# Performance work log

Measured on AMD Instinct MI355X. Metric: run time of the kernel, lower is better.

Reference implementation:

```python
import jax, jax.numpy as jnp
import numpy as np

# J6 incidence matrix for Plucker coordinates (constant buffer in the torch module)
_J6 = jnp.array([[0, 0, 0, 0, 0, 1],
                 [0, 0, 0, 0, -1, 0],
                 [0, 0, 0, 1, 0, 0],
                 [0, 0, 1, 0, 0, 0],
                 [0, -1, 0, 0, 0, 0],
                 [1, 0, 0, 0, 0, 0]], dtype=jnp.float32)

# combinations(range(4), 2) index pairs for the exterior product
_PI = np.array([0, 0, 0, 1, 1, 2])
_PJ = np.array([1, 2, 3, 2, 3, 3])


def plucker_lines(p1, p2):
    # p1, p2: (..., 4) -> normalized Plucker 6-vectors (..., 6)
    lines = p1[..., _PI] * p2[..., _PJ] - p1[..., _PJ] * p2[..., _PI]
    n = jnp.linalg.norm(lines, axis=-1, keepdims=True)
    return lines / jnp.maximum(n, 1e-12)


def setup_inputs() -> dict:
    key = jax.random.key(0)
    ks = jax.random.split(key, 6)
    B, T, D, H = 1, 2048, 1024, 16
    s = D ** -0.5
    x = jax.random.normal(ks[0], (B, T, D), jnp.float32)
    Wqkv = jax.random.normal(ks[1], (D, 3 * D), jnp.float32) * s
    bqkv = jnp.zeros((3 * D,), jnp.float32)
    W1p = jax.random.normal(ks[2], (D, 4 * H), jnp.float32) * s
    W2p = jax.random.normal(ks[3], (D, 4 * H), jnp.float32) * s
    plucker_scale = jnp.full((H,), 0.1, jnp.float32)
    Wout = jax.random.normal(ks[4], (D, D), jnp.float32) * s
    bout = jnp.zeros((D,), jnp.float32)
    return {"x": x, "Wqkv": Wqkv, "bqkv": bqkv, "W1p": W1p, "W2p": W2p,
            "plucker_scale": plucker_scale, "Wout": Wout, "bout": bout}


def reference(x, Wqkv, bqkv, W1p, W2p, plucker_scale, Wout, bout):
    B, T, D = x.shape
    H = plucker_scale.shape[0]
    dh = D // H

    qkv = (x @ Wqkv + bqkv).reshape(B, T, 3, H, dh)
    q = jnp.transpose(qkv[:, :, 0], (0, 2, 1, 3))  # [B,H,T,dh]
    k = jnp.transpose(qkv[:, :, 1], (0, 2, 1, 3))
    v = jnp.transpose(qkv[:, :, 2], (0, 2, 1, 3))

    std_logits = jnp.einsum('bhid,bhjd->bhij', q, k) * (dh ** -0.5)

    p1 = (x @ W1p).reshape(B, T, H, 4)
    p2 = (x @ W2p).reshape(B, T, H, 4)
    lines_h = jnp.transpose(plucker_lines(p1, p2), (0, 2, 1, 3))  # [B,H,T,6]
    Jlines = lines_h @ _J6.T                                       # [B,H,T,6]
    plucker_bias = jnp.einsum('bhic,bhjc->bhij', lines_h, Jlines)  # [B,H,T,T]

    logits = std_logits + plucker_bias * plucker_scale[None, :, None, None]
    causal = jnp.triu(jnp.ones((T, T), bool), 1)
    logits = jnp.where(causal[None, None], -jnp.inf, logits)
    attn = jax.nn.softmax(logits, axis=-1)

    out = jnp.einsum('bhij,bhjd->bhid', attn, v)
    out = jnp.transpose(out, (0, 2, 1, 3)).reshape(B, T, D)
    return out @ Wout + bout
```

## Files before the change

kernel.cpp:

```cpp
#include <hip/hip_runtime.h>

typedef unsigned short u16;
typedef unsigned int u32;
typedef __attribute__((ext_vector_type(8))) __bf16 bf16x8;
typedef __attribute__((ext_vector_type(4))) float f32x4;
typedef __attribute__((ext_vector_type(4))) u16 u16x4;

#define MFMA16(a, b, c) __builtin_amdgcn_mfma_f32_16x16x32_bf16((a), (b), (c), 0, 0, 0)

static __device__ __forceinline__ u16 f2b(float f) {
  union { float f; u32 u; } v; v.f = f;
  u32 u = v.u;
  return (u16)((u + 0x7FFFu + ((u >> 16) & 1u)) >> 16);
}

static __device__ __forceinline__ u32 pack2(float a, float b) {
  u32 r;
  asm("v_cvt_pk_bf16_f32 %0, %1, %2" : "=v"(r) : "v"(a), "v"(b));
  return r;
}

static __device__ __forceinline__ float exp2fast(float x) {
#if defined(__has_builtin) && __has_builtin(__builtin_amdgcn_exp2f)
  return __builtin_amdgcn_exp2f(x);
#else
  return __expf(x * 0.6931471805599453f);
#endif
}

static __device__ __forceinline__ void gload16(const u16* gp, u16* lp) {
  __builtin_amdgcn_global_load_lds((__attribute__((address_space(1))) void*)(u16*)gp,
                                   (__attribute__((address_space(3))) void*)lp, 16, 0, 0);
}

__global__ __launch_bounds__(256) void k_prep(const float* __restrict__ Wqkv, const float* __restrict__ Wout,
                                              const float* __restrict__ W1p, const float* __restrict__ W2p,
                                              const float* __restrict__ x,
                                              u16* __restrict__ WB, u16* __restrict__ WoT,
                                              u16* __restrict__ xb) {
  const int b = blockIdx.x;
  const int t = threadIdx.x;
  if (b < 4096) {
    __shared__ float tile[32][33];
    const float* src; u16* dst; int N, n0, k0;
    if (b < 3072) { src = Wqkv; dst = WB;  N = 3072; n0 = (b % 96) * 32; k0 = (b / 96) * 32; }
    else { const int bb = b - 3072; src = Wout; dst = WoT; N = 1024; n0 = (bb & 31) * 32; k0 = (bb >> 5) * 32; }
    const int r = t >> 3, c4 = (t & 7) << 2;
    const float4 in4 = *(const float4*)(src + (size_t)(k0 + r) * N + n0 + c4);
    tile[r][c4 + 0] = in4.x; tile[r][c4 + 1] = in4.y;
    tile[r][c4 + 2] = in4.z; tile[r][c4 + 3] = in4.w;
    __syncthreads();
    u16x4 o;
    o.x = f2b(tile[c4 + 0][r]); o.y = f2b(tile[c4 + 1][r]);
    o.z = f2b(tile[c4 + 2][r]); o.w = f2b(tile[c4 + 3][r]);
    *(u16x4*)(dst + (size_t)(n0 + r) * 1024 + k0 + c4) = o;
  } else if (b < 4608) {
    const int idx = (b - 4096) * 256 + t;
    const int j = idx >> 10, k = idx & 1023;
    const float v = (j < 64) ? W1p[(size_t)k * 64 + j] : W2p[(size_t)k * 64 + (j - 64)];
    WB[(size_t)3072 * 1024 + idx] = f2b(v);
  } else {
    const size_t idx = ((size_t)(b - 4608) * 256 + t) << 2;
    const float4 v = *(const float4*)(x + idx);
    u16x4 o; o.x = f2b(v.x); o.y = f2b(v.y); o.z = f2b(v.z); o.w = f2b(v.w);
    *(u16x4*)(xb + idx) = o;
  }
}

static __device__ __forceinline__ void gemm_core_128x64(const u16* __restrict__ A, const u16* __restrict__ B,
                                                        int brow, int bcol, int K,
                                                        u16* ldsA, u16* ldsB, f32x4 acc[4][2]) {
  const int tid = threadIdx.x;
  const int wave = tid >> 6, lane = tid & 63;
  const int wr = wave >> 1, wc = wave & 1;
  const int g = lane >> 4, l15 = lane & 15;

  for (int k0 = 0; k0 < K; k0 += 64) {
#pragma unroll
    for (int li = 0; li < 4; ++li) {
      const int f = li * 256 + wave * 64 + lane;
      const int row = f >> 3;
      const int slot = f & 7;
      const int gcol = ((slot ^ (row & 7)) << 3);
      gload16(A + (size_t)(brow + row) * K + k0 + gcol, ldsA + (size_t)(li * 256 + wave * 64) * 8);
    }
#pragma unroll
    for (int li = 0; li < 2; ++li) {
      const int f = li * 256 + wave * 64 + lane;
      const int row = f >> 3;
      const int slot = f & 7;
      const int gcol = ((slot ^ (row & 7)) << 3);
      gload16(B + (size_t)(bcol + row) * K + k0 + gcol, ldsB + (size_t)(li * 256 + wave * 64) * 8);
    }
    __syncthreads();
    bf16x8 af[4][2], bfr[2][2];
#pragma unroll
    for (int kk = 0; kk < 2; ++kk) {
#pragma unroll
      for (int m = 0; m < 4; ++m) {
        const int rowA = wr * 64 + m * 16 + l15;
        const int chA = (kk * 4 + g) ^ (rowA & 7);
        af[m][kk] = *(const bf16x8*)(ldsA + (size_t)rowA * 64 + chA * 8);
      }
#pragma unroll
      for (int n = 0; n < 2; ++n) {
        const int rowB = wc * 32 + n * 16 + l15;
        const int chB = (kk * 4 + g) ^ (rowB & 7);
        bfr[n][kk] = *(const bf16x8*)(ldsB + (size_t)rowB * 64 + chB * 8);
      }
    }
#pragma unroll
    for (int m = 0; m < 4; ++m)
#pragma unroll
      for (int n = 0; n < 2; ++n)
#pragma unroll
        for (int kk = 0; kk < 2; ++kk)
          acc[m][n] = MFMA16(af[m][kk], bfr[n][kk], acc[m][n]);
    __syncthreads();
  }
}

__global__ __launch_bounds__(256) void k_gemm_qkvp(const u16* __restrict__ xb, const u16* __restrict__ WB,
                                                   const float* __restrict__ bqkv,
                                                   u16* __restrict__ Qext, u16* __restrict__ Kext,
                                                   u16* __restrict__ Vt, float* __restrict__ P12) {
  __shared__ __align__(16) u16 ldsA[128 * 64];
  __shared__ __align__(16) u16 ldsB[64 * 64];
  const int bid = blockIdx.x;
  const int bn = bid % 50, bm = bid / 50;
  f32x4 acc[4][2];
#pragma unroll
  for (int m = 0; m < 4; ++m)
#pragma unroll
    for (int n = 0; n < 2; ++n) acc[m][n] = (f32x4){0.f, 0.f, 0.f, 0.f};
  gemm_core_128x64(xb, WB, bm * 128, bn * 64, 1024, ldsA, ldsB, acc);

  const int tid = threadIdx.x;
  const int wave = tid >> 6, lane = tid & 63;
  const int wr = wave >> 1, wc = wave & 1;
  const int g = lane >> 4, l15 = lane & 15;
  const int tbase = bm * 128 + wr * 64 + g * 4;
  const int cbase = bn * 64 + wc * 32 + l15;
#pragma unroll
  for (int m = 0; m < 4; ++m) {
#pragma unroll
    for (int n = 0; n < 2; ++n) {
      const int c = cbase + n * 16;
#pragma unroll
      for (int r = 0; r < 4; ++r) {
        const int t = tbase + m * 16 + r;
        float v = acc[m][n][r];
        if (c < 3072) {
          v += bqkv[c];
          const int sub = c >> 10;
          const int rem = c & 1023;
          const int hh = rem >> 6, d = rem & 63;
          if (sub == 0)      Qext[((size_t)hh * 2048 + t) * 96 + d] = f2b(v * 0.18033688f);
          else if (sub == 1) Kext[((size_t)hh * 2048 + t) * 96 + d] = f2b(v);
          else               Vt[(size_t)hh * 131072 + (size_t)(t >> 5) * 2048 + d * 32 + (t & 31)] = f2b(v);
        } else {
          P12[(size_t)t * 128 + (c - 3072)] = v;
        }
      }
    }
  }
}

__global__ __launch_bounds__(256) void k_lines(const float* __restrict__ P12, const float* __restrict__ pscale,
                                               u16* __restrict__ Qext, u16* __restrict__ Kext) {
  const int idx = blockIdx.x * 256 + threadIdx.x;
  const int t = idx >> 4, h = idx & 15;
  const float* p = P12 + (size_t)t * 128;
  const float a0 = p[h * 4 + 0], a1 = p[h * 4 + 1], a2 = p[h * 4 + 2], a3 = p[h * 4 + 3];
  const float b0 = p[64 + h * 4 + 0], b1 = p[64 + h * 4 + 1], b2 = p[64 + h * 4 + 2], b3 = p[64 + h * 4 + 3];
  float L0 = a0 * b1 - a1 * b0;
  float L1 = a0 * b2 - a2 * b0;
  float L2 = a0 * b3 - a3 * b0;
  float L3 = a1 * b2 - a2 * b1;
  float L4 = a1 * b3 - a3 * b1;
  float L5 = a2 * b3 - a3 * b2;
  const float nrm = sqrtf(L0 * L0 + L1 * L1 + L2 * L2 + L3 * L3 + L4 * L4 + L5 * L5);
  const float inv = 1.0f / fmaxf(nrm, 1e-12f);
  L0 *= inv; L1 *= inv; L2 *= inv; L3 *= inv; L4 *= inv; L5 *= inv;
  const float s = pscale[h] * 1.44269504f;
  u16* q = Qext + ((size_t)h * 2048 + t) * 96 + 64;
  u16* k = Kext + ((size_t)h * 2048 + t) * 96 + 64;
  q[0] = f2b(L0 * s); q[1] = f2b(L1 * s); q[2] = f2b(L2 * s);
  q[3] = f2b(L3 * s); q[4] = f2b(L4 * s); q[5] = f2b(L5 * s);
  k[0] = f2b(L5); k[1] = f2b(-L4); k[2] = f2b(L3);
  k[3] = f2b(L2); k[4] = f2b(-L1); k[5] = f2b(L0);
#pragma unroll
  for (int c = 6; c < 32; ++c) { q[c] = 0; k[c] = 0; }
}

__global__ __launch_bounds__(64) void k_attn(const u16* __restrict__ Qext, const u16* __restrict__ Kext,
                                             const u16* __restrict__ Vt, u16* __restrict__ AO) {
  const int bid = blockIdx.x;
  const int h = bid & 15;
  const int p = bid >> 4;
  const int lane = threadIdx.x;
  const int g = lane >> 4, l15 = lane & 15;
  const int q0A = p << 4;
  const int q0B = (127 - p) << 4;
  const int qgA = q0A + l15;
  const int qgB = q0B + l15;
  const int sA = (p >> 1) + 1;
  const int sB = ((127 - p) >> 1) + 1;
  const u16* Qh = Qext + (size_t)h * 2048 * 96;
  const u16* Kh = Kext + (size_t)h * 2048 * 96;
  const u16* Vh = Vt + (size_t)h * 131072;

  bf16x8 aqA[3], aqB[3];
#pragma unroll
  for (int ks = 0; ks < 3; ++ks) {
    aqA[ks] = *(const bf16x8*)(Qh + (size_t)qgA * 96 + ks * 32 + g * 8);
    aqB[ks] = *(const bf16x8*)(Qh + (size_t)qgB * 96 + ks * 32 + g * 8);
  }

  f32x4 accA[4], accB[4];
#pragma unroll
  for (int n = 0; n < 4; ++n) {
    accA[n] = (f32x4){0.f, 0.f, 0.f, 0.f};
    accB[n] = (f32x4){0.f, 0.f, 0.f, 0.f};
  }
  float lA = 0.f, lB = 0.f;

  const u16* Kbase = Kh + (size_t)l15 * 96 + g * 8;
  const int src0 = ((g & 1) << 5) + l15;
  const int src1 = src0 + 16;

  bf16x8 kX0[3], kX1[3], kY0[3], kY1[3];
#pragma unroll
  for (int ks = 0; ks < 3; ++ks) {
    kX0[ks] = *(const bf16x8*)(Kbase + ks * 32);
    kX1[ks] = *(const bf16x8*)(Kbase + 16 * 96 + ks * 32);
  }

#define GLUE(S0, S1, Q0S, QGS, LS, PBS)                                           \
  {                                                                               \
    if (jb + 31 > Q0S) {                                                          \
      _Pragma("unroll")                                                           \
      for (int r = 0; r < 4; ++r) {                                               \
        if (jb + g * 4 + r > QGS) S0[r] = -1e30f;                                 \
        if (jb + 16 + g * 4 + r > QGS) S1[r] = -1e30f;                            \
      }                                                                           \
    }                                                                             \
    _Pragma("unroll")                                                             \
    for (int r = 0; r < 4; ++r) {                                                 \
      S0[r] = exp2fast(S0[r]);                                                    \
      S1[r] = exp2fast(S1[r]);                                                    \
    }                                                                             \
    LS += ((S0[0] + S0[1]) + (S0[2] + S0[3])) + ((S1[0] + S1[1]) + (S1[2] + S1[3])); \
    const u32 w0 = pack2(S0[0], S0[1]);                                           \
    const u32 w1 = pack2(S0[2], S0[3]);                                           \
    const u32 w2 = pack2(S1[0], S1[1]);                                           \
    const u32 w3 = pack2(S1[2], S1[3]);                                           \
    const u32 a0 = (u32)__shfl((int)w0, src0);                                    \
    const u32 a1 = (u32)__shfl((int)w2, src0);                                    \
    const u32 b0 = (u32)__shfl((int)w1, src0);                                    \
    const u32 b1 = (u32)__shfl((int)w3, src0);                                    \
    const u32 c0 = (u32)__shfl((int)w0, src1);                                    \
    const u32 c1 = (u32)__shfl((int)w2, src1);                                    \
    const u32 d0 = (u32)__shfl((int)w1, src1);                                    \
    const u32 d1 = (u32)__shfl((int)w3, src1);                                    \
    PBS.u[0] = (g & 2) ? a1 : a0;                                                 \
    PBS.u[1] = (g & 2) ? b1 : b0;                                                 \
    PBS.u[2] = (g & 2) ? c1 : c0;                                                 \
    PBS.u[3] = (g & 2) ? d1 : d0;                                                 \
  }

#define ATTN_STEP(KC0, KC1, KN0, KN1)                                             \
  {                                                                               \
    const int jb = jt * 32;                                                       \
    const bool actA = (jt < sA);                                                  \
    f32x4 SB0 = (f32x4){0.f, 0.f, 0.f, 0.f}, SB1 = (f32x4){0.f, 0.f, 0.f, 0.f};   \
    f32x4 SA0 = (f32x4){0.f, 0.f, 0.f, 0.f}, SA1 = (f32x4){0.f, 0.f, 0.f, 0.f};   \
    __builtin_amdgcn_s_setprio(1);                                                \
    _Pragma("unroll")                                                             \
    for (int ks = 0; ks < 3; ++ks) {                                              \
      SB0 = MFMA16(KC0[ks], aqB[ks], SB0);                                        \
      SB1 = MFMA16(KC1[ks], aqB[ks], SB1);                                        \
    }                                                                             \
    if (actA) {                                                                   \
      _Pragma("unroll")                                                           \
      for (int ks = 0; ks < 3; ++ks) {                                            \
        SA0 = MFMA16(KC0[ks], aqA[ks], SA0);                                      \
        SA1 = MFMA16(KC1[ks], aqA[ks], SA1);                                      \
      }                                                                           \
    }                                                                             \
    __builtin_amdgcn_s_setprio(0);                                                \
    bf16x8 av[4];            \
    _Pragma("unroll")                                                             \
    for (int n = 0; n < 4; ++n)                                                   \
      av[n] = *(const bf16x8*)(Vh + (size_t)jb * 64 + (n * 16 + l15) * 32 + g * 8); \
    const int jbn = (jt + 1 < sB) ? jb + 32 : jb;          \
    const u16* kp = Kbase + (size_t)jbn * 96;                                     \
    _Pragma("unroll")                                                             \
    for (int ks = 0; ks < 3; ++ks) {                                              \
      KN0[ks] = *(const bf16x8*)(kp + ks * 32);                                   \
      KN1[ks] = *(const bf16x8*)(kp + 16 * 96 + ks * 32);                         \
    }                                                                             \
    union { u32 u[4]; bf16x8 bv; } pbB, pbA;                                      \
    GLUE(SB0, SB1, q0B, qgB, lB, pbB);                                            \
    if (actA) GLUE(SA0, SA1, q0A, qgA, lA, pbA);                                  \
    __builtin_amdgcn_s_setprio(1);                                                \
    _Pragma("unroll")                                                             \
    for (int n = 0; n < 4; ++n) accB[n] = MFMA16(av[n], pbB.bv, accB[n]);         \
    if (actA) {                                                                   \
      _Pragma("unroll")                                                           \
      for (int n = 0; n < 4; ++n) accA[n] = MFMA16(av[n], pbA.bv, accA[n]);       \
    }                                                                             \
    __builtin_amdgcn_s_setprio(0);                                                \
  }

  int jt = 0;
  for (;;) {
    ATTN_STEP(kX0, kX1, kY0, kY1);
    if (++jt >= sB) break;
    ATTN_STEP(kY0, kY1, kX0, kX1);
    if (++jt >= sB) break;
  }
#undef ATTN_STEP
#undef GLUE

  lA += __shfl_xor(lA, 16);
  lA += __shfl_xor(lA, 32);
  lB += __shfl_xor(lB, 16);
  lB += __shfl_xor(lB, 32);
  const float invA = 1.0f / lA;
  const float invB = 1.0f / lB;
  u32* dstA = (u32*)(AO + (size_t)qgA * 1024 + h * 64 + g * 4);
  u32* dstB = (u32*)(AO + (size_t)qgB * 1024 + h * 64 + g * 4);
#pragma unroll
  for (int n = 0; n < 4; ++n) {
    dstA[n * 8 + 0] = pack2(accA[n][0] * invA, accA[n][1] * invA);
    dstA[n * 8 + 1] = pack2(accA[n][2] * invA, accA[n][3] * invA);
    dstB[n * 8 + 0] = pack2(accB[n][0] * invB, accB[n][1] * invB);
    dstB[n * 8 + 1] = pack2(accB[n][2] * invB, accB[n][3] * invB);
  }
}

__global__ __launch_bounds__(256) void k_gemm_out(const u16* __restrict__ AO, const u16* __restrict__ WoT,
                                                  const float* __restrict__ bout, float* __restrict__ out) {
  __shared__ __align__(16) u16 ldsA[128 * 64];
  __shared__ __align__(16) u16 ldsB[64 * 64];
  const int bid = blockIdx.x;
  const int bn = bid & 15, bm = bid >> 4;
  f32x4 acc[4][2];
#pragma unroll
  for (int m = 0; m < 4; ++m)
#pragma unroll
    for (int n = 0; n < 2; ++n) acc[m][n] = (f32x4){0.f, 0.f, 0.f, 0.f};
  gemm_core_128x64(AO, WoT, bm * 128, bn * 64, 1024, ldsA, ldsB, acc);

  const int tid = threadIdx.x;
  const int wave = tid >> 6, lane = tid & 63;
  const int wr = wave >> 1, wc = wave & 1;
  const int g = lane >> 4, l15 = lane & 15;
  const int tbase = bm * 128 + wr * 64 + g * 4;
  const int cbase = bn * 64 + wc * 32 + l15;
#pragma unroll
  for (int m = 0; m < 4; ++m)
#pragma unroll
    for (int n = 0; n < 2; ++n) {
      const int c = cbase + n * 16;
      const float bb = bout[c];
#pragma unroll
      for (int r = 0; r < 4; ++r) {
        const int t = tbase + m * 16 + r;
        out[(size_t)t * 1024 + c] = acc[m][n][r] + bb;
      }
    }
}

extern "C" void kernel_launch(void* const* d_in, const int* in_sizes, int n_in,
                              void* d_out, int out_size, void* d_ws, size_t ws_size,
                              hipStream_t stream) {
  const float* x      = (const float*)d_in[0];
  const float* Wqkv   = (const float*)d_in[1];
  const float* bqkv   = (const float*)d_in[2];
  const float* W1p    = (const float*)d_in[3];
  const float* W2p    = (const float*)d_in[4];
  const float* pscale = (const float*)d_in[5];
  const float* Wout   = (const float*)d_in[6];
  const float* bout   = (const float*)d_in[7];
  float* out = (float*)d_out;

  char* ws = (char*)d_ws;
  u16*   WB    = (u16*)(ws + 0);
  u16*   WoT   = (u16*)(ws + 6553600);
  u16*   xb    = (u16*)(ws + 8650752);
  u16*   Qext  = (u16*)(ws + 12845056);
  u16*   Kext  = (u16*)(ws + 19136512);
  u16*   Vt    = (u16*)(ws + 25427968);
  float* P12   = (float*)(ws + 29622272);
  u16*   AO    = (u16*)(ws + 30670848);

  k_prep<<<6656, 256, 0, stream>>>(Wqkv, Wout, W1p, W2p, x, WB, WoT, xb);
  k_gemm_qkvp<<<800, 256, 0, stream>>>(xb, WB, bqkv, Qext, Kext, Vt, P12);
  k_lines<<<128, 256, 0, stream>>>(P12, pscale, Qext, Kext);
  k_attn<<<1024, 64, 0, stream>>>(Qext, Kext, Vt, AO);
  k_gemm_out<<<256, 256, 0, stream>>>(AO, WoT, bout, out);
}
```

Before: 102.0 us.

## Software-pipeline QK^T one tile ahead in attention and shrink output GEMM tiles

The attention loop now computes the QK^T scores for tile j+1 while tile j's softmax and PV MFMAs run. It also prefetches K two tiles ahead and V one tile ahead into double-buffered registers, hiding MFMA and load latency behind the exp/shuffle glue. Separately, the output GEMM moves from a 128x64 tile to a 128x32 tile with its own inline loop, doubling the grid to 512 blocks for better CU occupancy. The costs are higher register pressure in the attention kernel and more redundant A-tile loads in the GEMM.

```diff
diff --git a/kernel.cpp b/kernel.cpp
--- a/kernel.cpp
+++ b/kernel.cpp
@@ -226,14 +226,36 @@
   float lA = 0.f, lB = 0.f;
 
   const u16* Kbase = Kh + (size_t)l15 * 96 + g * 8;
+  const u16* Vlane = Vh + (size_t)l15 * 32 + g * 8;
   const int src0 = ((g & 1) << 5) + l15;
   const int src1 = src0 + 16;
 
   bf16x8 kX0[3], kX1[3], kY0[3], kY1[3];
-#pragma unroll
-  for (int ks = 0; ks < 3; ++ks) {
-    kX0[ks] = *(const bf16x8*)(Kbase + ks * 32);
-    kX1[ks] = *(const bf16x8*)(Kbase + 16 * 96 + ks * 32);
+  bf16x8 avX[4], avY[4];
+  f32x4 SA0c, SA1c, SB0c, SB1c, SA0n, SA1n, SB0n, SB1n;
+
+  {
+#pragma unroll
+    for (int ks = 0; ks < 3; ++ks) {
+      kX0[ks] = *(const bf16x8*)(Kbase + ks * 32);
+      kX1[ks] = *(const bf16x8*)(Kbase + 16 * 96 + ks * 32);
+    }
+    SB0c = (f32x4){0.f, 0.f, 0.f, 0.f}; SB1c = SB0c; SA0c = SB0c; SA1c = SB0c;
+#pragma unroll
+    for (int ks = 0; ks < 3; ++ks) {
+      SB0c = MFMA16(kX0[ks], aqB[ks], SB0c);
+      SB1c = MFMA16(kX1[ks], aqB[ks], SB1c);
+      SA0c = MFMA16(kX0[ks], aqA[ks], SA0c);
+      SA1c = MFMA16(kX1[ks], aqA[ks], SA1c);
+    }
+    const u16* kp = Kbase + (size_t)((1 < sB) ? 1 : 0) * 32 * 96;
+#pragma unroll
+    for (int ks = 0; ks < 3; ++ks) {
+      kY0[ks] = *(const bf16x8*)(kp + ks * 32);
+      kY1[ks] = *(const bf16x8*)(kp + 16 * 96 + ks * 32);
+    }
+#pragma unroll
+    for (int n = 0; n < 4; ++n) avX[n] = *(const bf16x8*)(Vlane + n * 512);
   }
 
 #define GLUE(S0, S1, Q0S, QGS, LS, PBS)                                           \
@@ -269,55 +291,60 @@
     PBS.u[3] = (g & 2) ? d1 : d0;                                                 \
   }
 
-#define ATTN_STEP(KC0, KC1, KN0, KN1)                                             \
+#define ATTN_STEP(SA0C, SA1C, SB0C, SB1C, SA0N, SA1N, SB0N, SB1N, KN0, KN1, KL0, KL1, AVC, AVN) \
   {                                                                               \
     const int jb = jt * 32;                                                       \
-    const bool actA = (jt < sA);                                                  \
-    f32x4 SB0 = (f32x4){0.f, 0.f, 0.f, 0.f}, SB1 = (f32x4){0.f, 0.f, 0.f, 0.f};   \
-    f32x4 SA0 = (f32x4){0.f, 0.f, 0.f, 0.f}, SA1 = (f32x4){0.f, 0.f, 0.f, 0.f};   \
+    const int jn1 = (jt + 1 < sB) ? jt + 1 : jt;                                  \
+    const int jn2 = (jt + 2 < sB) ? jt + 2 : jt;                                  \
+                                     \
+    SB0N = (f32x4){0.f, 0.f, 0.f, 0.f}; SB1N = SB0N;                              \
     __builtin_amdgcn_s_setprio(1);                                                \
     _Pragma("unroll")                                                             \
     for (int ks = 0; ks < 3; ++ks) {                                              \
-      SB0 = MFMA16(KC0[ks], aqB[ks], SB0);                                        \
-      SB1 = MFMA16(KC1[ks], aqB[ks], SB1);                                        \
-    }                                                                             \
+      SB0N = MFMA16(KN0[ks], aqB[ks], SB0N);                                      \
+      SB1N = MFMA16(KN1[ks], aqB[ks], SB1N);                                      \
+    }                                                                             \
+    if (jt + 1 < sA) {                                                            \
+      SA0N = (f32x4){0.f, 0.f, 0.f, 0.f}; SA1N = SA0N;                            \
+      _Pragma("unroll")                                                           \
+      for (int ks = 0; ks < 3; ++ks) {                                            \
+        SA0N = MFMA16(KN0[ks], aqA[ks], SA0N);                                    \
+        SA1N = MFMA16(KN1[ks], aqA[ks], SA1N);                                    \
+      }                                                                           \
+    }                                                                             \
+    __builtin_amdgcn_s_setprio(0);                                                \
+                                                         \
+    const u16* kp = Kbase + (size_t)jn2 * 32 * 96;                                \
+    _Pragma("unroll")                                                             \
+    for (int ks = 0; ks < 3; ++ks) {                                              \
+      KL0[ks] = *(const bf16x8*)(kp + ks * 32);                                   \
+      KL1[ks] = *(const bf16x8*)(kp + 16 * 96 + ks * 32);                         \
+    }                                                                             \
+                                                         \
+    _Pragma("unroll")                                                             \
+    for (int n = 0; n < 4; ++n)                                                   \
+      AVN[n] = *(const bf16x8*)(Vlane + (size_t)jn1 * 2048 + n * 512);            \
+                                                      \
+    union { u32 u[4]; bf16x8 bv; } pbB, pbA;                                      \
+    GLUE(SB0C, SB1C, q0B, qgB, lB, pbB);                                          \
+    const bool actA = (jt < sA);                                                  \
+    if (actA) GLUE(SA0C, SA1C, q0A, qgA, lA, pbA);                                \
+                                                 \
+    __builtin_amdgcn_s_setprio(1);                                                \
+    _Pragma("unroll")                                                             \
+    for (int n = 0; n < 4; ++n) accB[n] = MFMA16(AVC[n], pbB.bv, accB[n]);        \
     if (actA) {                                                                   \
       _Pragma("unroll")                                                           \
-      for (int ks = 0; ks < 3; ++ks) {                                            \
-        SA0 = MFMA16(KC0[ks], aqA[ks], SA0);                                      \
-        SA1 = MFMA16(KC1[ks], aqA[ks], SA1);                                      \
-      }                                                                           \
-    }                                                                             \
-    __builtin_amdgcn_s_setprio(0);                                                \
-    bf16x8 av[4];            \
-    _Pragma("unroll")                                                             \
-    for (int n = 0; n < 4; ++n)                                                   \
-      av[n] = *(const bf16x8*)(Vh + (size_t)jb * 64 + (n * 16 + l15) * 32 + g * 8); \
-    const int jbn = (jt + 1 < sB) ? jb + 32 : jb;          \
-    const u16* kp = Kbase + (size_t)jbn * 96;                                     \
-    _Pragma("unroll")                                                             \
-    for (int ks = 0; ks < 3; ++ks) {                                              \
-      KN0[ks] = *(const bf16x8*)(kp + ks * 32);                                   \
-      KN1[ks] = *(const bf16x8*)(kp + 16 * 96 + ks * 32);                         \
-    }                                                                             \
-    union { u32 u[4]; bf16x8 bv; } pbB, pbA;                                      \
-    GLUE(SB0, SB1, q0B, qgB, lB, pbB);                                            \
-    if (actA) GLUE(SA0, SA1, q0A, qgA, lA, pbA);                                  \
-    __builtin_amdgcn_s_setprio(1);                                                \
-    _Pragma("unroll")                                                             \
-    for (int n = 0; n < 4; ++n) accB[n] = MFMA16(av[n], pbB.bv, accB[n]);         \
-    if (actA) {                                                                   \
-      _Pragma("unroll")                                                           \
-      for (int n = 0; n < 4; ++n) accA[n] = MFMA16(av[n], pbA.bv, accA[n]);       \
+      for (int n = 0; n < 4; ++n) accA[n] = MFMA16(AVC[n], pbA.bv, accA[n]);      \
     }                                                                             \
     __builtin_amdgcn_s_setprio(0);                                                \
   }
 
   int jt = 0;
   for (;;) {
-    ATTN_STEP(kX0, kX1, kY0, kY1);
+    ATTN_STEP(SA0c, SA1c, SB0c, SB1c, SA0n, SA1n, SB0n, SB1n, kY0, kY1, kX0, kX1, avX, avY);
     if (++jt >= sB) break;
-    ATTN_STEP(kY0, kY1, kX0, kX1);
+    ATTN_STEP(SA0n, SA1n, SB0n, SB1n, SA0c, SA1c, SB0c, SB1c, kX0, kX1, kY0, kY1, avY, avX);
     if (++jt >= sB) break;
   }
 #undef ATTN_STEP
@@ -343,33 +370,65 @@
 __global__ __launch_bounds__(256) void k_gemm_out(const u16* __restrict__ AO, const u16* __restrict__ WoT,
                                                   const float* __restrict__ bout, float* __restrict__ out) {
   __shared__ __align__(16) u16 ldsA[128 * 64];
-  __shared__ __align__(16) u16 ldsB[64 * 64];
+  __shared__ __align__(16) u16 ldsB[32 * 64];
   const int bid = blockIdx.x;
-  const int bn = bid & 15, bm = bid >> 4;
-  f32x4 acc[4][2];
-#pragma unroll
-  for (int m = 0; m < 4; ++m)
-#pragma unroll
-    for (int n = 0; n < 2; ++n) acc[m][n] = (f32x4){0.f, 0.f, 0.f, 0.f};
-  gemm_core_128x64(AO, WoT, bm * 128, bn * 64, 1024, ldsA, ldsB, acc);
-
+  const int bn = bid & 31, bm = bid >> 5;
   const int tid = threadIdx.x;
   const int wave = tid >> 6, lane = tid & 63;
   const int wr = wave >> 1, wc = wave & 1;
   const int g = lane >> 4, l15 = lane & 15;
+
+  f32x4 acc[4];
+#pragma unroll
+  for (int m = 0; m < 4; ++m) acc[m] = (f32x4){0.f, 0.f, 0.f, 0.f};
+
+  for (int k0 = 0; k0 < 1024; k0 += 64) {
+#pragma unroll
+    for (int li = 0; li < 4; ++li) {
+      const int f = li * 256 + wave * 64 + lane;
+      const int row = f >> 3;
+      const int slot = f & 7;
+      const int gcol = ((slot ^ (row & 7)) << 3);
+      gload16(AO + (size_t)(bm * 128 + row) * 1024 + k0 + gcol, ldsA + (size_t)(li * 256 + wave * 64) * 8);
+    }
+    {
+      const int f = wave * 64 + lane;
+      const int row = f >> 3;
+      const int slot = f & 7;
+      const int gcol = ((slot ^ (row & 7)) << 3);
+      gload16(WoT + (size_t)(bn * 32 + row) * 1024 + k0 + gcol, ldsB + (size_t)(wave * 64) * 8);
+    }
+    __syncthreads();
+    bf16x8 af[4][2], bfr[2];
+#pragma unroll
+    for (int kk = 0; kk < 2; ++kk) {
+#pragma unroll
+      for (int m = 0; m < 4; ++m) {
+        const int rowA = wr * 64 + m * 16 + l15;
+        const int chA = (kk * 4 + g) ^ (rowA & 7);
+        af[m][kk] = *(const bf16x8*)(ldsA + (size_t)rowA * 64 + chA * 8);
+      }
+      const int rowB = wc * 16 + l15;
+      const int chB = (kk * 4 + g) ^ (rowB & 7);
+      bfr[kk] = *(const bf16x8*)(ldsB + (size_t)rowB * 64 + chB * 8);
+    }
+#pragma unroll
+    for (int m = 0; m < 4; ++m)
+#pragma unroll
+      for (int kk = 0; kk < 2; ++kk)
+        acc[m] = MFMA16(af[m][kk], bfr[kk], acc[m]);
+    __syncthreads();
+  }
+
   const int tbase = bm * 128 + wr * 64 + g * 4;
-  const int cbase = bn * 64 + wc * 32 + l15;
+  const int c = bn * 32 + wc * 16 + l15;
+  const float bb = bout[c];
 #pragma unroll
   for (int m = 0; m < 4; ++m)
 #pragma unroll
-    for (int n = 0; n < 2; ++n) {
-      const int c = cbase + n * 16;
-      const float bb = bout[c];
-#pragma unroll
-      for (int r = 0; r < 4; ++r) {
-        const int t = tbase + m * 16 + r;
-        out[(size_t)t * 1024 + c] = acc[m][n][r] + bb;
-      }
+    for (int r = 0; r < 4; ++r) {
+      const int t = tbase + m * 16 + r;
+      out[(size_t)t * 1024 + c] = acc[m][r] + bb;
     }
 }
 
@@ -400,5 +459,5 @@
   k_gemm_qkvp<<<800, 256, 0, stream>>>(xb, WB, bqkv, Qext, Kext, Vt, P12);
   k_lines<<<128, 256, 0, stream>>>(P12, pscale, Qext, Kext);
   k_attn<<<1024, 64, 0, stream>>>(Qext, Kext, Vt, AO);
-  k_gemm_out<<<256, 256, 0, stream>>>(AO, WoT, bout, out);
-}
+  k_gemm_out<<<512, 256, 0, stream>>>(AO, WoT, bout, out);
+}
```

Measured after the change: 97.21 us. -4.7%, faster.
